# Performance work log

Measured on AMD Instinct MI355X. Metric: run time of the kernel, lower is better.

## Reference

```python
import jax, jax.numpy as jnp
import numpy as np

B, S, E, H = 4, 2048, 1024, 16
D = E // H  # head dim


def setup_inputs() -> dict:
    key = jax.random.key(0)
    ks = jax.random.split(key, 6)
    sc = 1.0 / np.sqrt(E)
    return {
        "x":  jax.random.normal(ks[0], (B, S, E), dtype=jnp.float32),
        "Wk": jax.random.normal(ks[1], (E, E), dtype=jnp.float32) * sc,
        "Wq": jax.random.normal(ks[2], (E, E), dtype=jnp.float32) * sc,
        "Wv": jax.random.normal(ks[3], (E, E), dtype=jnp.float32) * sc,
        "Wo": jax.random.normal(ks[4], (E, E), dtype=jnp.float32) * sc,
        "bo": jax.random.normal(ks[5], (E,), dtype=jnp.float32) * sc,
    }


def reference(x, Wk, Wq, Wv, Wo, bo):
    b, s, e = x.shape
    # torch Linear: y = x @ W.T (weights are [out, in])
    K = x @ Wk.T
    Q = x @ Wq.T
    _V_unused = x @ Wv.T  # computed in source but discarded (V = Q.view bug)
    # split heads: [b, s, H, D] -> [b, H, s, D]
    Kh = K.reshape(b, s, H, D).transpose(0, 2, 1, 3)
    Qh = Q.reshape(b, s, H, D).transpose(0, 2, 1, 3)
    Vh = Qh  # faithful to source: V = Q.view(...)
    # scaled dot product, scaled by sqrt(embedding_size) as in source
    scores = jnp.einsum('bhqd,bhkd->bhqk', Qh, Kh) / jnp.sqrt(jnp.float32(e))
    causal = jnp.tril(jnp.ones((s, s), dtype=bool))
    scores = jnp.where(causal, scores, -jnp.inf)
    probs = jax.nn.softmax(scores, axis=-1)
    attn = jnp.einsum('bhqk,bhkd->bhqd', probs, Vh)
    attn = attn.transpose(0, 2, 1, 3).reshape(b, s, e)
    return attn @ Wo.T + bo
```

## Files before the change

kernel.cpp:

```cpp
#include <hip/hip_runtime.h>
#include <hip/hip_bf16.h>

#define PB 4
#define PS 2048
#define PE 1024
#define PH 16
#define PD 64

typedef __attribute__((ext_vector_type(8))) short bf16x8;
typedef __attribute__((ext_vector_type(4))) float f32x4;
typedef const __attribute__((address_space(1))) unsigned int* gas_t;
typedef __attribute__((address_space(3))) unsigned int* las_t;

__device__ __forceinline__ unsigned short f2bf(float f) {
  union { float f; unsigned int u; } v;
  v.f = f;
  unsigned int u = v.u;
  u += 0x7fffu + ((u >> 16) & 1u);
  return (unsigned short)(u >> 16);
}

__device__ __forceinline__ f32x4 mfma16(bf16x8 a, bf16x8 b, f32x4 c) {
  return __builtin_amdgcn_mfma_f32_16x16x32_bf16(a, b, c, 0, 0, 0);
}

#define CVT_GROUPS ((PB * PS * PE + 3 * PE * PE) / 4)
#define CVT_BLOCKS (CVT_GROUPS / 256)
__global__ __launch_bounds__(256) void cvt_kernel(
    const float* __restrict__ x, const float* __restrict__ wk,
    const float* __restrict__ wq, const float* __restrict__ wo,
    unsigned short* __restrict__ xb, unsigned short* __restrict__ wkb,
    unsigned short* __restrict__ wqb, unsigned short* __restrict__ wob) {
  const long long NX = (long long)PB * PS * PE;
  const long long NW = (long long)PE * PE;
  long long i = ((long long)blockIdx.x * 256 + threadIdx.x) * 4;
  const float* src;
  unsigned short* dst;
  long long off;
  if (i < NX)               { src = x;  dst = xb;  off = i; }
  else if (i < NX + NW)     { src = wk; dst = wkb; off = i - NX; }
  else if (i < NX + 2 * NW) { src = wq; dst = wqb; off = i - NX - NW; }
  else                      { src = wo; dst = wob; off = i - NX - 2 * NW; }
  float4 v = *(const float4*)(src + off);
  ushort4 o;
  o.x = f2bf(v.x); o.y = f2bf(v.y); o.z = f2bf(v.z); o.w = f2bf(v.w);
  *(ushort4*)(dst + off) = o;
}

__global__ __launch_bounds__(256) void gemm_qk(
    const unsigned short* __restrict__ A, const unsigned short* __restrict__ Bq,
    const unsigned short* __restrict__ Bk,
    unsigned short* __restrict__ QT, unsigned short* __restrict__ Kb) {
  const int K = PE, N = PE;
  __shared__ __attribute__((aligned(16))) unsigned short As[128 * 64];
  __shared__ __attribute__((aligned(16))) unsigned short Bqs[128 * 64];
  __shared__ __attribute__((aligned(16))) unsigned short Bks[128 * 64];
  const int tid = threadIdx.x;
  const int wave = tid >> 6, lane = tid & 63;
  const int quad = lane >> 4, ln = lane & 15;
  const int m0 = blockIdx.y * 128, n0 = blockIdx.x * 128;
  const int wm = (wave >> 1) * 64, wn = (wave & 1) * 64;

  f32x4 aq[4][4], ak[4][4];
#pragma unroll
  for (int i = 0; i < 4; ++i)
#pragma unroll
    for (int j = 0; j < 4; ++j)
#pragma unroll
      for (int r = 0; r < 4; ++r) { aq[i][j][r] = 0.f; ak[i][j][r] = 0.f; }

  for (int k0 = 0; k0 < K; k0 += 64) {
#pragma unroll
    for (int it = 0; it < 4; ++it) {
      const int idx = it * 256 + tid;
      const int row = idx >> 3, ch = idx & 7;
      const int gch = ch ^ (row & 7);
      __builtin_amdgcn_global_load_lds(
          (gas_t)(const void*)(A + (size_t)(m0 + row) * K + k0 + gch * 8),
          (las_t)(void*)((char*)As + idx * 16), 16, 0, 0);
      __builtin_amdgcn_global_load_lds(
          (gas_t)(const void*)(Bq + (size_t)(n0 + row) * K + k0 + gch * 8),
          (las_t)(void*)((char*)Bqs + idx * 16), 16, 0, 0);
      __builtin_amdgcn_global_load_lds(
          (gas_t)(const void*)(Bk + (size_t)(n0 + row) * K + k0 + gch * 8),
          (las_t)(void*)((char*)Bks + idx * 16), 16, 0, 0);
    }
    __syncthreads();
#pragma unroll
    for (int kc = 0; kc < 2; ++kc) {
      bf16x8 af[4], bqf[4], bkf[4];
#pragma unroll
      for (int t = 0; t < 4; ++t) {
        const int ra = wm + t * 16 + ln;
        const int rb = wn + t * 16 + ln;
        af[t]  = *(const bf16x8*)(As  + ra * 64 + ((kc * 4 + quad) ^ (ra & 7)) * 8);
        bqf[t] = *(const bf16x8*)(Bqs + rb * 64 + ((kc * 4 + quad) ^ (rb & 7)) * 8);
        bkf[t] = *(const bf16x8*)(Bks + rb * 64 + ((kc * 4 + quad) ^ (rb & 7)) * 8);
      }
#pragma unroll
      for (int mt = 0; mt < 4; ++mt)
#pragma unroll
        for (int nt = 0; nt < 4; ++nt) {
          aq[mt][nt] = mfma16(af[mt], bqf[nt], aq[mt][nt]);
          ak[mt][nt] = mfma16(bkf[nt], af[mt], ak[mt][nt]);
        }
    }
    __syncthreads();
  }

  const float CEXP = 0.045084220f;
#pragma unroll
  for (int mt = 0; mt < 4; ++mt) {
#pragma unroll
    for (int nt = 0; nt < 4; ++nt) {
      {
        const int row = m0 + wm + mt * 16 + quad * 4;
        const int col = n0 + wn + nt * 16 + ln;
        const int b = row >> 11, s = row & 2047;
        const int h = col >> 6, d = col & 63;
        ushort4 ov;
        ov.x = f2bf(aq[mt][nt][0]); ov.y = f2bf(aq[mt][nt][1]);
        ov.z = f2bf(aq[mt][nt][2]); ov.w = f2bf(aq[mt][nt][3]);
        *(ushort4*)(QT + (((size_t)(b * PH + h) * PD + d) * PS + s)) = ov;
      }
      {
        const int krow = m0 + wm + mt * 16 + ln;
        const int kcol = n0 + wn + nt * 16 + quad * 4;
        ushort4 kv;
        kv.x = f2bf(ak[mt][nt][0] * CEXP); kv.y = f2bf(ak[mt][nt][1] * CEXP);
        kv.z = f2bf(ak[mt][nt][2] * CEXP); kv.w = f2bf(ak[mt][nt][3] * CEXP);
        *(ushort4*)(Kb + (size_t)krow * N + kcol) = kv;
      }
    }
  }
}

__global__ __launch_bounds__(256) void gemm_out(
    const unsigned short* __restrict__ A, const unsigned short* __restrict__ Bm,
    const float* __restrict__ bias, float* __restrict__ Cf) {
  const int K = PE, N = PE;
  __shared__ __attribute__((aligned(16))) unsigned short As[128 * 64];
  __shared__ __attribute__((aligned(16))) unsigned short Bs[128 * 64];
  const int tid = threadIdx.x;
  const int wave = tid >> 6, lane = tid & 63;
  const int quad = lane >> 4, ln = lane & 15;
  const int m0 = blockIdx.y * 128, n0 = blockIdx.x * 128;
  const int wm = (wave >> 1) * 64, wn = (wave & 1) * 64;

  f32x4 acc[4][4];
#pragma unroll
  for (int i = 0; i < 4; ++i)
#pragma unroll
    for (int j = 0; j < 4; ++j)
#pragma unroll
      for (int r = 0; r < 4; ++r) acc[i][j][r] = 0.f;

  for (int k0 = 0; k0 < K; k0 += 64) {
#pragma unroll
    for (int it = 0; it < 4; ++it) {
      const int idx = it * 256 + tid;
      const int row = idx >> 3, ch = idx & 7;
      const int gch = ch ^ (row & 7);
      __builtin_amdgcn_global_load_lds(
          (gas_t)(const void*)(A + (size_t)(m0 + row) * K + k0 + gch * 8),
          (las_t)(void*)((char*)As + idx * 16), 16, 0, 0);
      __builtin_amdgcn_global_load_lds(
          (gas_t)(const void*)(Bm + (size_t)(n0 + row) * K + k0 + gch * 8),
          (las_t)(void*)((char*)Bs + idx * 16), 16, 0, 0);
    }
    __syncthreads();
#pragma unroll
    for (int kc = 0; kc < 2; ++kc) {
      bf16x8 af[4], bfr[4];
#pragma unroll
      for (int t = 0; t < 4; ++t) {
        const int ra = wm + t * 16 + ln;
        const int rb = wn + t * 16 + ln;
        af[t]  = *(const bf16x8*)(As + ra * 64 + ((kc * 4 + quad) ^ (ra & 7)) * 8);
        bfr[t] = *(const bf16x8*)(Bs + rb * 64 + ((kc * 4 + quad) ^ (rb & 7)) * 8);
      }
#pragma unroll
      for (int mt = 0; mt < 4; ++mt)
#pragma unroll
        for (int nt = 0; nt < 4; ++nt)
          acc[mt][nt] = mfma16(bfr[nt], af[mt], acc[mt][nt]);
    }
    __syncthreads();
  }

#pragma unroll
  for (int mt = 0; mt < 4; ++mt) {
#pragma unroll
    for (int nt = 0; nt < 4; ++nt) {
      const int row  = m0 + wm + mt * 16 + ln;
      const int colb = n0 + wn + nt * 16 + quad * 4;
      const float4 bv = *(const float4*)(bias + colb);
      float4 ov;
      ov.x = acc[mt][nt][0] + bv.x; ov.y = acc[mt][nt][1] + bv.y;
      ov.z = acc[mt][nt][2] + bv.z; ov.w = acc[mt][nt][3] + bv.w;
      *(float4*)(Cf + (size_t)row * N + colb) = ov;
    }
  }
}

__global__ __launch_bounds__(256) void attn_kernel(
    const unsigned short* __restrict__ QT,
    const unsigned short* __restrict__ Kb,
    unsigned short* __restrict__ Ab) {
  __shared__ __attribute__((aligned(16))) unsigned short Ks[64 * 64];
  __shared__ __attribute__((aligned(16))) unsigned short Vs[64 * 64];
  __shared__ __attribute__((aligned(16))) unsigned short Ps[4][16 * 72];

  const int tid = threadIdx.x;
  const int wave = tid >> 6, lane = tid & 63;
  const int quad = lane >> 4, ln = lane & 15;
  const int h = blockIdx.y, b = blockIdx.z;
  const size_t hoff  = ((size_t)b * PS) * PE + (size_t)h * PD;
  const size_t hofft = ((size_t)(b * PH + h) * PD) * PS;
  const int srow = tid >> 3, sch = tid & 7;

  for (int pass = 0; pass < 2; ++pass) {
    const int qc = pass ? (int)blockIdx.x : 31 - (int)blockIdx.x;
    const int qw0 = qc * 64 + wave * 16;

    bf16x8 qfr[2];
#pragma unroll
    for (int c = 0; c < 2; ++c) {
      union { unsigned short u[8]; bf16x8 v; } tmp;
#pragma unroll
      for (int j = 0; j < 8; ++j)
        tmp.u[j] = QT[hofft + (size_t)(c * 32 + quad * 8 + j) * PS + qw0 + ln];
      qfr[c] = tmp.v;
    }

    f32x4 o[4];
    float psum = 0.f;
#pragma unroll
    for (int td = 0; td < 4; ++td)
#pragma unroll
      for (int r = 0; r < 4; ++r) o[td][r] = 0.f;

    const int ktend = qc + 1;
    for (int kt = 0; kt < ktend; ++kt) {
      const int k0 = kt * 64;

#pragma unroll
      for (int r = 0; r < 2; ++r) {
        const int row = r * 32 + srow;
        const int gch = sch ^ (row & 7);
        __builtin_amdgcn_global_load_lds(
            (gas_t)(const void*)(Kb + hoff + (size_t)(k0 + row) * PE + gch * 8),
            (las_t)(void*)((char*)Ks + (r * 256 + tid) * 16), 16, 0, 0);
        __builtin_amdgcn_global_load_lds(
            (gas_t)(const void*)(QT + hofft + (size_t)row * PS + k0 + gch * 8),
            (las_t)(void*)((char*)Vs + (r * 256 + tid) * 16), 16, 0, 0);
      }
      __syncthreads();

      f32x4 sacc[4];
#pragma unroll
      for (int mk = 0; mk < 4; ++mk)
#pragma unroll
        for (int r = 0; r < 4; ++r) sacc[mk][r] = 0.f;
      __builtin_amdgcn_s_setprio(1);
#pragma unroll
      for (int c = 0; c < 2; ++c) {
        const int ch = ((c * 4 + quad) ^ (ln & 7)) * 8;
        bf16x8 kf[4];
#pragma unroll
        for (int mk = 0; mk < 4; ++mk)
          kf[mk] = *(const bf16x8*)(Ks + (mk * 16 + ln) * 64 + ch);
#pragma unroll
        for (int mk = 0; mk < 4; ++mk)
          sacc[mk] = mfma16(kf[mk], qfr[c], sacc[mk]);
      }
      __builtin_amdgcn_s_setprio(0);

      const bool edge = (k0 + 63) > qw0;
#pragma unroll
      for (int mk = 0; mk < 4; ++mk) {
        float p[4];
#pragma unroll
        for (int r = 0; r < 4; ++r)
          p[r] = __builtin_amdgcn_exp2f(sacc[mk][r]);
        if (edge) {
          const int qg = qw0 + ln;
#pragma unroll
          for (int r = 0; r < 4; ++r) {
            const int kg = k0 + mk * 16 + quad * 4 + r;
            p[r] = (kg <= qg) ? p[r] : 0.f;
          }
        }
        psum += (p[0] + p[1]) + (p[2] + p[3]);
        union { __hip_bfloat162 h2; unsigned int u; } u01, u23;
        u01.h2 = __float22bfloat162_rn(float2{p[0], p[1]});
        u23.h2 = __float22bfloat162_rn(float2{p[2], p[3]});
        *(uint2*)(&Ps[wave][ln * 72 + mk * 16 + quad * 4]) =
            uint2{u01.u, u23.u};
      }

      __builtin_amdgcn_s_setprio(1);
#pragma unroll
      for (int c = 0; c < 2; ++c) {
        const int ch = ((c * 4 + quad) ^ (ln & 7)) * 8;
        bf16x8 pf = *(const bf16x8*)(&Ps[wave][ln * 72 + c * 32 + quad * 8]);
#pragma unroll
        for (int td = 0; td < 4; ++td) {
          bf16x8 vfd = *(const bf16x8*)(Vs + (td * 16 + ln) * 64 + ch);
          o[td] = mfma16(pf, vfd, o[td]);
        }
      }
      __builtin_amdgcn_s_setprio(0);
      __syncthreads();
    }

    psum += __shfl_xor(psum, 16, 64);
    psum += __shfl_xor(psum, 32, 64);
    float invq[4];
#pragma unroll
    for (int r = 0; r < 4; ++r)
      invq[r] = 1.f / __shfl(psum, quad * 4 + r, 64);

#pragma unroll
    for (int r = 0; r < 4; ++r) {
      const int qg = qw0 + quad * 4 + r;
#pragma unroll
      for (int td = 0; td < 4; ++td)
        Ab[hoff + (size_t)qg * PE + td * 16 + ln] =
            f2bf(o[td][r] * invq[r]);
    }
  }
}

extern "C" void kernel_launch(void* const* d_in, const int* in_sizes, int n_in,
                              void* d_out, int out_size, void* d_ws, size_t ws_size,
                              hipStream_t stream) {
  (void)in_sizes; (void)n_in; (void)out_size; (void)ws_size;
  const float* x  = (const float*)d_in[0];
  const float* Wk = (const float*)d_in[1];
  const float* Wq = (const float*)d_in[2];
  const float* Wo = (const float*)d_in[4];
  const float* bo = (const float*)d_in[5];
  float* out = (float*)d_out;

  char* ws = (char*)d_ws;
  unsigned short* xb  = (unsigned short*)(ws);
  unsigned short* wkb = (unsigned short*)(ws + (16u << 20));
  unsigned short* wqb = (unsigned short*)(ws + (18u << 20));
  unsigned short* wob = (unsigned short*)(ws + (20u << 20));
  unsigned short* QT  = (unsigned short*)(ws + (22u << 20));
  unsigned short* Kb  = (unsigned short*)(ws + (38u << 20));
  unsigned short* Ab  = xb;

  const int M = PB * PS;

  cvt_kernel<<<dim3(CVT_BLOCKS), dim3(256), 0, stream>>>(
      x, Wk, Wq, Wo, xb, wkb, wqb, wob);

  gemm_qk<<<dim3(PE / 128, M / 128), dim3(256), 0, stream>>>(
      xb, wqb, wkb, QT, Kb);

  attn_kernel<<<dim3(16, PH, PB), dim3(256), 0, stream>>>(QT, Kb, Ab);

  gemm_out<<<dim3(PE / 128, M / 128), dim3(256), 0, stream>>>(
      Ab, wob, bo, out);
}
```

Before: 257.3 us.

## Split fused Q/K GEMM across grid z and halve output GEMM M-tile

The fused Q/K projection kernel, which held two 4x4 accumulator sets and three LDS tiles per block, is split so each block computes either Q or K, selected by blockIdx.z. This doubles the grid and roughly halves accumulator registers and LDS per block, which should raise occupancy and wave count. In exchange, each block now reloads the shared x tile once per output. The output GEMM's M tile shrinks from 128 to 64, doubling its block count to fill more CUs, at the cost of lower per-block data reuse of the Wo tile.

Measured after the change: 246.4 us. 1.04x faster.

```diff
diff --git a/kernel.cpp b/kernel.cpp
--- a/kernel.cpp
+++ b/kernel.cpp
@@ -47,27 +47,28 @@
   *(ushort4*)(dst + off) = o;
 }
 
-__global__ __launch_bounds__(256) void gemm_qk(
+__global__ __launch_bounds__(256) void gemm_qknt(
     const unsigned short* __restrict__ A, const unsigned short* __restrict__ Bq,
     const unsigned short* __restrict__ Bk,
     unsigned short* __restrict__ QT, unsigned short* __restrict__ Kb) {
   const int K = PE, N = PE;
   __shared__ __attribute__((aligned(16))) unsigned short As[128 * 64];
-  __shared__ __attribute__((aligned(16))) unsigned short Bqs[128 * 64];
-  __shared__ __attribute__((aligned(16))) unsigned short Bks[128 * 64];
+  __shared__ __attribute__((aligned(16))) unsigned short Bs[128 * 64];
   const int tid = threadIdx.x;
   const int wave = tid >> 6, lane = tid & 63;
   const int quad = lane >> 4, ln = lane & 15;
   const int m0 = blockIdx.y * 128, n0 = blockIdx.x * 128;
   const int wm = (wave >> 1) * 64, wn = (wave & 1) * 64;
-
-  f32x4 aq[4][4], ak[4][4];
+  const int isK = blockIdx.z;
+  const unsigned short* __restrict__ Bsrc = isK ? Bk : Bq;
+
+  f32x4 acc[4][4];
 #pragma unroll
   for (int i = 0; i < 4; ++i)
 #pragma unroll
     for (int j = 0; j < 4; ++j)
 #pragma unroll
-      for (int r = 0; r < 4; ++r) { aq[i][j][r] = 0.f; ak[i][j][r] = 0.f; }
+      for (int r = 0; r < 4; ++r) acc[i][j][r] = 0.f;
 
   for (int k0 = 0; k0 < K; k0 += 64) {
 #pragma unroll
@@ -79,59 +80,64 @@
           (gas_t)(const void*)(A + (size_t)(m0 + row) * K + k0 + gch * 8),
           (las_t)(void*)((char*)As + idx * 16), 16, 0, 0);
       __builtin_amdgcn_global_load_lds(
-          (gas_t)(const void*)(Bq + (size_t)(n0 + row) * K + k0 + gch * 8),
-          (las_t)(void*)((char*)Bqs + idx * 16), 16, 0, 0);
-      __builtin_amdgcn_global_load_lds(
-          (gas_t)(const void*)(Bk + (size_t)(n0 + row) * K + k0 + gch * 8),
-          (las_t)(void*)((char*)Bks + idx * 16), 16, 0, 0);
+          (gas_t)(const void*)(Bsrc + (size_t)(n0 + row) * K + k0 + gch * 8),
+          (las_t)(void*)((char*)Bs + idx * 16), 16, 0, 0);
     }
     __syncthreads();
 #pragma unroll
     for (int kc = 0; kc < 2; ++kc) {
-      bf16x8 af[4], bqf[4], bkf[4];
+      bf16x8 af[4], bfr[4];
 #pragma unroll
       for (int t = 0; t < 4; ++t) {
         const int ra = wm + t * 16 + ln;
         const int rb = wn + t * 16 + ln;
-        af[t]  = *(const bf16x8*)(As  + ra * 64 + ((kc * 4 + quad) ^ (ra & 7)) * 8);
-        bqf[t] = *(const bf16x8*)(Bqs + rb * 64 + ((kc * 4 + quad) ^ (rb & 7)) * 8);
-        bkf[t] = *(const bf16x8*)(Bks + rb * 64 + ((kc * 4 + quad) ^ (rb & 7)) * 8);
-      }
-#pragma unroll
-      for (int mt = 0; mt < 4; ++mt)
-#pragma unroll
-        for (int nt = 0; nt < 4; ++nt) {
-          aq[mt][nt] = mfma16(af[mt], bqf[nt], aq[mt][nt]);
-          ak[mt][nt] = mfma16(bkf[nt], af[mt], ak[mt][nt]);
-        }
+        af[t]  = *(const bf16x8*)(As + ra * 64 + ((kc * 4 + quad) ^ (ra & 7)) * 8);
+        bfr[t] = *(const bf16x8*)(Bs + rb * 64 + ((kc * 4 + quad) ^ (rb & 7)) * 8);
+      }
+      if (!isK) {
+#pragma unroll
+        for (int mt = 0; mt < 4; ++mt)
+#pragma unroll
+          for (int nt = 0; nt < 4; ++nt)
+            acc[mt][nt] = mfma16(af[mt], bfr[nt], acc[mt][nt]);
+      } else {
+#pragma unroll
+        for (int mt = 0; mt < 4; ++mt)
+#pragma unroll
+          for (int nt = 0; nt < 4; ++nt)
+            acc[mt][nt] = mfma16(bfr[nt], af[mt], acc[mt][nt]);
+      }
     }
     __syncthreads();
   }
 
   const float CEXP = 0.045084220f;
-#pragma unroll
-  for (int mt = 0; mt < 4; ++mt) {
-#pragma unroll
-    for (int nt = 0; nt < 4; ++nt) {
-      {
+  if (!isK) {
+#pragma unroll
+    for (int mt = 0; mt < 4; ++mt)
+#pragma unroll
+      for (int nt = 0; nt < 4; ++nt) {
         const int row = m0 + wm + mt * 16 + quad * 4;
         const int col = n0 + wn + nt * 16 + ln;
         const int b = row >> 11, s = row & 2047;
         const int h = col >> 6, d = col & 63;
         ushort4 ov;
-        ov.x = f2bf(aq[mt][nt][0]); ov.y = f2bf(aq[mt][nt][1]);
-        ov.z = f2bf(aq[mt][nt][2]); ov.w = f2bf(aq[mt][nt][3]);
+        ov.x = f2bf(acc[mt][nt][0]); ov.y = f2bf(acc[mt][nt][1]);
+        ov.z = f2bf(acc[mt][nt][2]); ov.w = f2bf(acc[mt][nt][3]);
         *(ushort4*)(QT + (((size_t)(b * PH + h) * PD + d) * PS + s)) = ov;
       }
-      {
+  } else {
+#pragma unroll
+    for (int mt = 0; mt < 4; ++mt)
+#pragma unroll
+      for (int nt = 0; nt < 4; ++nt) {
         const int krow = m0 + wm + mt * 16 + ln;
         const int kcol = n0 + wn + nt * 16 + quad * 4;
         ushort4 kv;
-        kv.x = f2bf(ak[mt][nt][0] * CEXP); kv.y = f2bf(ak[mt][nt][1] * CEXP);
-        kv.z = f2bf(ak[mt][nt][2] * CEXP); kv.w = f2bf(ak[mt][nt][3] * CEXP);
+        kv.x = f2bf(acc[mt][nt][0] * CEXP); kv.y = f2bf(acc[mt][nt][1] * CEXP);
+        kv.z = f2bf(acc[mt][nt][2] * CEXP); kv.w = f2bf(acc[mt][nt][3] * CEXP);
         *(ushort4*)(Kb + (size_t)krow * N + kcol) = kv;
       }
-    }
   }
 }
 
@@ -139,17 +145,17 @@
     const unsigned short* __restrict__ A, const unsigned short* __restrict__ Bm,
     const float* __restrict__ bias, float* __restrict__ Cf) {
   const int K = PE, N = PE;
-  __shared__ __attribute__((aligned(16))) unsigned short As[128 * 64];
+  __shared__ __attribute__((aligned(16))) unsigned short As[64 * 64];
   __shared__ __attribute__((aligned(16))) unsigned short Bs[128 * 64];
   const int tid = threadIdx.x;
   const int wave = tid >> 6, lane = tid & 63;
   const int quad = lane >> 4, ln = lane & 15;
-  const int m0 = blockIdx.y * 128, n0 = blockIdx.x * 128;
-  const int wm = (wave >> 1) * 64, wn = (wave & 1) * 64;
-
-  f32x4 acc[4][4];
-#pragma unroll
-  for (int i = 0; i < 4; ++i)
+  const int m0 = blockIdx.y * 64, n0 = blockIdx.x * 128;
+  const int wm = (wave >> 1) * 32, wn = (wave & 1) * 64;
+
+  f32x4 acc[2][4];
+#pragma unroll
+  for (int i = 0; i < 2; ++i)
 #pragma unroll
     for (int j = 0; j < 4; ++j)
 #pragma unroll
@@ -157,13 +163,19 @@
 
   for (int k0 = 0; k0 < K; k0 += 64) {
 #pragma unroll
-    for (int it = 0; it < 4; ++it) {
+    for (int it = 0; it < 2; ++it) {
       const int idx = it * 256 + tid;
       const int row = idx >> 3, ch = idx & 7;
       const int gch = ch ^ (row & 7);
       __builtin_amdgcn_global_load_lds(
           (gas_t)(const void*)(A + (size_t)(m0 + row) * K + k0 + gch * 8),
           (las_t)(void*)((char*)As + idx * 16), 16, 0, 0);
+    }
+#pragma unroll
+    for (int it = 0; it < 4; ++it) {
+      const int idx = it * 256 + tid;
+      const int row = idx >> 3, ch = idx & 7;
+      const int gch = ch ^ (row & 7);
       __builtin_amdgcn_global_load_lds(
           (gas_t)(const void*)(Bm + (size_t)(n0 + row) * K + k0 + gch * 8),
           (las_t)(void*)((char*)Bs + idx * 16), 16, 0, 0);
@@ -171,16 +183,19 @@
     __syncthreads();
 #pragma unroll
     for (int kc = 0; kc < 2; ++kc) {
-      bf16x8 af[4], bfr[4];
+      bf16x8 af[2], bfr[4];
+#pragma unroll
+      for (int t = 0; t < 2; ++t) {
+        const int ra = wm + t * 16 + ln;
+        af[t] = *(const bf16x8*)(As + ra * 64 + ((kc * 4 + quad) ^ (ra & 7)) * 8);
+      }
 #pragma unroll
       for (int t = 0; t < 4; ++t) {
-        const int ra = wm + t * 16 + ln;
         const int rb = wn + t * 16 + ln;
-        af[t]  = *(const bf16x8*)(As + ra * 64 + ((kc * 4 + quad) ^ (ra & 7)) * 8);
         bfr[t] = *(const bf16x8*)(Bs + rb * 64 + ((kc * 4 + quad) ^ (rb & 7)) * 8);
       }
 #pragma unroll
-      for (int mt = 0; mt < 4; ++mt)
+      for (int mt = 0; mt < 2; ++mt)
 #pragma unroll
         for (int nt = 0; nt < 4; ++nt)
           acc[mt][nt] = mfma16(bfr[nt], af[mt], acc[mt][nt]);
@@ -189,7 +204,7 @@
   }
 
 #pragma unroll
-  for (int mt = 0; mt < 4; ++mt) {
+  for (int mt = 0; mt < 2; ++mt) {
 #pragma unroll
     for (int nt = 0; nt < 4; ++nt) {
       const int row  = m0 + wm + mt * 16 + ln;
@@ -357,11 +372,11 @@
   cvt_kernel<<<dim3(CVT_BLOCKS), dim3(256), 0, stream>>>(
       x, Wk, Wq, Wo, xb, wkb, wqb, wob);
 
-  gemm_qk<<<dim3(PE / 128, M / 128), dim3(256), 0, stream>>>(
+  gemm_qknt<<<dim3(PE / 128, M / 128, 2), dim3(256), 0, stream>>>(
       xb, wqb, wkb, QT, Kb);
 
   attn_kernel<<<dim3(16, PH, PB), dim3(256), 0, stream>>>(QT, Kb, Ab);
 
-  gemm_out<<<dim3(PE / 128, M / 128), dim3(256), 0, stream>>>(
+  gemm_out<<<dim3(PE / 128, M / 64), dim3(256), 0, stream>>>(
       Ab, wob, bo, out);
 }
```
